# Kernel optimization log

Measured on AMD Instinct MI355X. Metric: run time of the kernel, lower is better.

The kernel has to match this reference:

```python
import jax, jax.numpy as jnp
import numpy as np

B, N, D = 32, 1024, 256
NHID = 512
NHID_HALF = NHID // 2
NCLASS = 2


def _xavier(key, shape):
    fan_in, fan_out = shape
    lim = float(np.sqrt(6.0 / (fan_in + fan_out)))
    return jax.random.uniform(key, shape, jnp.float32, -lim, lim)


def setup_inputs() -> dict:
    key = jax.random.key(0)
    ks = jax.random.split(key, 10)
    x = jax.random.normal(ks[0], (B, N, D), jnp.float32)
    adj = jax.random.uniform(ks[1], (B, N, N), jnp.float32)
    adj = adj / jnp.sum(adj, axis=-1, keepdims=True)  # row-normalized (mean aggregation)
    # GraphConv weights: shape (2*in_dim, out_dim) due to concat([x, agg(x)])
    W1 = _xavier(ks[2], (2 * D, NHID))
    b1 = jnp.zeros((NHID,), jnp.float32)
    W2 = _xavier(ks[3], (2 * NHID, NHID))
    b2 = jnp.zeros((NHID,), jnp.float32)
    W3 = _xavier(ks[4], (2 * NHID, NHID_HALF))
    b3 = jnp.zeros((NHID_HALF,), jnp.float32)
    W4 = _xavier(ks[5], (2 * NHID_HALF, NHID_HALF))
    b4 = jnp.zeros((NHID_HALF,), jnp.float32)
    # classifier: Linear(256,256) + PReLU(256) + Linear(256,2)
    cW1 = _xavier(ks[6], (NHID_HALF, NHID_HALF))
    cb1 = jnp.zeros((NHID_HALF,), jnp.float32)
    alpha = jnp.full((NHID_HALF,), 0.25, jnp.float32)
    cW2 = _xavier(ks[7], (NHID_HALF, NCLASS))
    cb2 = jnp.zeros((NCLASS,), jnp.float32)
    return {"x": x, "adj": adj, "W1": W1, "b1": b1, "W2": W2, "b2": b2,
            "W3": W3, "b3": b3, "W4": W4, "b4": b4,
            "cW1": cW1, "cb1": cb1, "alpha": alpha, "cW2": cW2, "cb2": cb2}


def _graphconv(x, adj, W, b):
    agg = jnp.einsum('bnm,bmd->bnd', adj, x)          # mean aggregation (adj row-normalized)
    cat = jnp.concatenate([x, agg], axis=-1)          # [B, N, 2*d]
    return jax.nn.relu(jnp.einsum('bnd,df->bnf', cat, W) + b)


def reference(x, adj, W1, b1, W2, b2, W3, b3, W4, b4, cW1, cb1, alpha, cW2, cb2):
    h = _graphconv(x, adj, W1, b1)
    h = _graphconv(h, adj, W2, b2)
    h = _graphconv(h, adj, W3, b3)
    h = _graphconv(h, adj, W4, b4)
    # classifier MLP with channel-wise PReLU
    h = jnp.einsum('bnd,df->bnf', h, cW1) + cb1
    h = jnp.where(h > 0, h, alpha * h)
    pred = jnp.einsum('bnd,df->bnf', h, cW2) + cb2
    return pred
```

## Files before the change

kernel.cpp:

```cpp
#include <hip/hip_runtime.h>

typedef short v8s __attribute__((ext_vector_type(8)));
typedef _Float16 v8h __attribute__((ext_vector_type(8)));
typedef float v4f __attribute__((ext_vector_type(4)));

#define BMT 128
#define BNT 128
#define BKT 32

__device__ __forceinline__ unsigned short f2bf(float f) {
    unsigned int u = __float_as_uint(f);
    u += 0x7fff + ((u >> 16) & 1);
    return (unsigned short)(u >> 16);
}
__device__ __forceinline__ unsigned short f2h(float f) {
    union { _Float16 h; unsigned short u; } c;
    c.h = (_Float16)f;
    return c.u;
}
__device__ __forceinline__ float h2f(unsigned short v) {
    union { unsigned short u; _Float16 h; } c;
    c.u = v;
    return (float)c.h;
}
__device__ __forceinline__ v8h as_h(v8s x) {
    union { v8s s; v8h h; } c;
    c.s = x;
    return c.h;
}

union U128 { unsigned short s[8]; uint4 v; };

__device__ __forceinline__ void gld16(const unsigned short* g, unsigned short* l) {
    __builtin_amdgcn_global_load_lds((const __attribute__((address_space(1))) void*)g,
                                     (__attribute__((address_space(3))) void*)l, 16, 0, 0);
}

__global__ __launch_bounds__(256) void split_f16(const float* __restrict__ x,
                                                 unsigned short* __restrict__ o, int n4) {
    int i = blockIdx.x * 256 + threadIdx.x;
    if (i < n4) {
        float4 f = ((const float4*)x)[i];
        float fv[4] = {f.x, f.y, f.z, f.w};
        ushort4 h;
        unsigned short* hp = (unsigned short*)&h;
#pragma unroll
        for (int j = 0; j < 4; ++j) hp[j] = f2h(fv[j]);
        ((ushort4*)o)[i] = h;
    }
}

__global__ __launch_bounds__(256) void split_hi(const float* __restrict__ x,
                                                unsigned short* __restrict__ oh, int n4) {
    int i = blockIdx.x * 256 + threadIdx.x;
    if (i < n4) {
        float4 f = ((const float4*)x)[i];
        float fv[4] = {f.x, f.y, f.z, f.w};
        ushort4 h;
        unsigned short* hp = (unsigned short*)&h;
#pragma unroll
        for (int j = 0; j < 4; ++j) hp[j] = f2bf(fv[j]);
        ((ushort4*)oh)[i] = h;
    }
}

__global__ __launch_bounds__(256) void tsplit16(const float* __restrict__ W,
                                                unsigned short* __restrict__ th, int R, int C) {
    int e = blockIdx.x * 256 + threadIdx.x;
    if (e < R * C) {
        int k = e / C, n = e - k * C;
        th[(size_t)n * R + k] = f2h(W[e]);
    }
}

__global__ __launch_bounds__(256) void transp_x(const float* __restrict__ src,
                                                unsigned short* __restrict__ th, int d) {
    __shared__ unsigned int lds[64 * 66];
    const int t = threadIdx.x;
    const int mt = blockIdx.x, ft = blockIdx.y, z = blockIdx.z;
    const int r = t >> 3, c8 = (t & 7) * 8;
#pragma unroll
    for (int half = 0; half < 2; ++half) {
        int rr = r + half * 32;
        size_t grow = (size_t)z * 1024 + mt * 64 + rr;
        const float* xs = src + grow * d + ft * 64 + c8;
        float4 f0 = *(const float4*)xs;
        float4 f1 = *(const float4*)(xs + 4);
        float fv[8] = {f0.x, f0.y, f0.z, f0.w, f1.x, f1.y, f1.z, f1.w};
#pragma unroll
        for (int j = 0; j < 8; ++j)
            lds[rr * 66 + c8 + j] = f2bf(fv[j]);
    }
    __syncthreads();
    const int f = t >> 3, m0 = (t & 7) * 8;
#pragma unroll
    for (int half = 0; half < 2; ++half) {
        int ff = f + half * 32;
        U128 uh;
#pragma unroll
        for (int j = 0; j < 8; ++j)
            uh.s[j] = (unsigned short)lds[(m0 + j) * 66 + ff];
        size_t orow = ((size_t)z * d + ft * 64 + ff) * 1024 + mt * 64 + m0;
        *(uint4*)(th + orow) = uh.v;
    }
}

template <int ACT, bool TWO, int AMODE, int DT, bool WRT>
__global__ __launch_bounds__(256) void gemm128(
    const void* a1, const unsigned short* __restrict__ a2,
    int K1, int K2,
    const unsigned short* __restrict__ b_, int ldb,
    const float* __restrict__ bias, const float* __restrict__ alpha,
    unsigned short* __restrict__ o_, int Nout,
    unsigned short* __restrict__ th,
    size_t aZ, size_t bZ, int cZRows,
    int nblk, int mBits)
{
    constexpr int LA = (AMODE == 0) ? 32 : 40;
    constexpr int LB = 32;
    __shared__ __align__(16) unsigned short Ash[BMT * LA];
    __shared__ __align__(16) unsigned short Bsh[BNT * LB];

    const int t = threadIdx.x;
    const int lane = t & 63, wave = t >> 6;
    const int wm = wave >> 1, wn = wave & 1;
    const int l15 = lane & 15, quad = lane >> 4;

    const int bx = blockIdx.x;
    const int low3 = bx & 7, rest = bx >> 3;
    const int nIdx = rest % nblk, g = rest / nblk;
    const int grp = g * 8 + low3;
    const int m0 = (grp & ((1 << mBits) - 1)) * BMT;
    const int zb = grp >> mBits;
    const int n0 = nIdx * BNT;

    const unsigned short* bhz = b_ + (size_t)zb * bZ;

    v4f acc[4][4] = {};

    const int nch = TWO ? 2 : 1;
    for (int ch = 0; ch < nch; ++ch) {
        const int K = (TWO && ch) ? K2 : K1;
        const int kr0 = (TWO && ch) ? K1 : 0;
        const unsigned short* ah = nullptr;
        const float* af = nullptr;
        if constexpr (AMODE == 0)
            ah = (ch ? a2 : (const unsigned short*)a1) + (size_t)zb * aZ;
        else
            af = (const float*)a1 + (size_t)zb * aZ;

        for (int kk = 0; kk < K; kk += BKT) {
            __syncthreads();
            if constexpr (AMODE == 0) {
#pragma unroll
                for (int i = 0; i < 2; ++i) {
                    int s = i * 256 + t;
                    int row = s >> 2;
                    int cg = (s & 3) ^ ((s >> 3) & 3);
                    size_t go = (size_t)(m0 + row) * K + kk + cg * 8;
                    int ls = (i * 256 + (t & ~63)) * 8;
                    gld16(ah + go, &Ash[ls]);
                }
            } else {
#pragma unroll
                for (int i = 0; i < 2; ++i) {
                    int cid = i * 256 + t;
                    int row = cid >> 2, c = cid & 3;
                    const float* src = af + (size_t)(m0 + row) * K + kk + c * 8;
                    float4 f0 = *(const float4*)src;
                    float4 f1 = *(const float4*)(src + 4);
                    float fv[8] = {f0.x, f0.y, f0.z, f0.w, f1.x, f1.y, f1.z, f1.w};
                    U128 uh;
#pragma unroll
                    for (int j = 0; j < 8; ++j) uh.s[j] = f2bf(fv[j]);
                    *(uint4*)&Ash[row * LA + c * 8] = uh.v;
                }
            }
#pragma unroll
            for (int i = 0; i < 2; ++i) {
                int s = i * 256 + t;
                int row = s >> 2;
                int cg = (s & 3) ^ ((s >> 3) & 3);
                size_t go = (size_t)(n0 + row) * ldb + kr0 + kk + cg * 8;
                int ls = (i * 256 + (t & ~63)) * 8;
                gld16(bhz + go, &Bsh[ls]);
            }
            __syncthreads();
            v8s ahf[4];
#pragma unroll
            for (int mi = 0; mi < 4; ++mi) {
                int row = wm * 64 + mi * 16 + l15;
                int off;
                if constexpr (AMODE == 0) off = row * LA + ((quad ^ ((row >> 1) & 3)) * 8);
                else                      off = row * LA + quad * 8;
                ahf[mi] = *(const v8s*)&Ash[off];
            }
#pragma unroll
            for (int ni = 0; ni < 4; ++ni) {
                int row = wn * 64 + ni * 16 + l15;
                int off = row * LB + ((quad ^ ((row >> 1) & 3)) * 8);
                v8s bhf = *(const v8s*)&Bsh[off];
#pragma unroll
                for (int mi = 0; mi < 4; ++mi) {
                    if constexpr (DT == 0)
                        acc[mi][ni] = __builtin_amdgcn_mfma_f32_16x16x32_bf16(ahf[mi], bhf, acc[mi][ni], 0, 0, 0);
                    else
                        acc[mi][ni] = __builtin_amdgcn_mfma_f32_16x16x32_f16(as_h(ahf[mi]), as_h(bhf), acc[mi][ni], 0, 0, 0);
                }
            }
        }
    }

    const size_t crow0 = (size_t)zb * cZRows + m0;
#pragma unroll
    for (int ni = 0; ni < 4; ++ni) {
        int n = n0 + wn * 64 + ni * 16 + l15;
        float bv = (ACT > 0) ? bias[n] : 0.f;
        float av = (ACT == 2) ? alpha[n] : 0.f;
#pragma unroll
        for (int mi = 0; mi < 4; ++mi) {
#pragma unroll
            for (int r = 0; r < 4; ++r) {
                int m = wm * 64 + mi * 16 + quad * 4 + r;
                float v = acc[mi][ni][r] + bv;
                if (ACT == 1) v = v > 0.f ? v : 0.f;
                if (ACT == 2) v = v > 0.f ? v : av * v;
                acc[mi][ni][r] = v;
                o_[(crow0 + m) * (size_t)Nout + n] = f2h(v);
            }
        }
    }

    if constexpr (WRT) {
        const int zbT = m0 >> 10;
        const int mloc0 = (m0 & 1023) + wm * 64;
#pragma unroll
        for (int ni = 0; ni < 4; ++ni) {
            int f = n0 + wn * 64 + ni * 16 + l15;
            size_t rowb = (((size_t)zbT * Nout + f) << 10) + mloc0;
#pragma unroll
            for (int mi = 0; mi < 4; ++mi) {
                ushort4 u;
                unsigned short* up = (unsigned short*)&u;
#pragma unroll
                for (int r = 0; r < 4; ++r) up[r] = f2bf(acc[mi][ni][r]);
                *(ushort4*)(th + rowb + mi * 16 + quad * 4) = u;
            }
        }
    }
}

template <int ACT, bool TWO, int DT, bool WRT, int BN2>
__global__ __launch_bounds__(512, 2) void gemm256(
    const unsigned short* __restrict__ a1, const unsigned short* __restrict__ a2,
    int K1, int K2,
    const unsigned short* __restrict__ b_, int ldb,
    const float* __restrict__ bias, const float* __restrict__ alpha,
    unsigned short* __restrict__ o_, int Nout,
    unsigned short* __restrict__ th,
    size_t aZ, size_t bZ, int cZRows,
    int nblk, int mBits)
{
    constexpr int ASLOT = 256 * 32;
    constexpr int BSLOT = BN2 * 32;
    constexpr int SLOT  = ASLOT + BSLOT;
    constexpr int LPT   = 2 + BN2 / 128;
    constexpr int WN    = BN2 / 64;
    constexpr int WM    = 8 / WN;
    constexpr int MREP  = 16 / WM;
    __shared__ __align__(16) unsigned short lds[4 * SLOT];

    const int t = threadIdx.x;
    const int lane = t & 63, wave = t >> 6;
    const int wm = wave / WN, wn = wave % WN;
    const int l15 = lane & 15, quad = lane >> 4;

    const int bx = blockIdx.x;
    const int low3 = bx & 7, rest = bx >> 3;
    const int nIdx = rest % nblk, g = rest / nblk;
    const int grp = g * 8 + low3;
    const int m0 = (grp & ((1 << mBits) - 1)) * 256;
    const int zb = grp >> mBits;
    const int n0 = nIdx * BN2;

    const unsigned short* A1 = a1 + (size_t)zb * aZ;
    const unsigned short* A2p = TWO ? (a2 + (size_t)zb * aZ) : nullptr;
    const unsigned short* B = b_ + (size_t)zb * bZ;

    const int NT1 = K1 >> 5;
    const int NTtot = NT1 + (TWO ? (K2 >> 5) : 0);

    auto stage = [&](int tt) {
        unsigned short* slot = &lds[(tt & 3) * SLOT];
        const unsigned short* abase;
        int astr;
        if constexpr (TWO) {
            if (tt >= NT1) { abase = A2p + ((size_t)(tt - NT1) << 5); astr = K2; }
            else           { abase = A1 + ((size_t)tt << 5); astr = K1; }
        } else {
            abase = A1 + ((size_t)tt << 5); astr = K1;
        }
#pragma unroll
        for (int i = 0; i < 2; ++i) {
            int s = i * 512 + t;
            int row = s >> 2;
            int cg = (s & 3) ^ ((s >> 3) & 3);
            gld16(abase + (size_t)(m0 + row) * astr + cg * 8,
                  &slot[(i * 512 + (t & ~63)) * 8]);
        }
        const unsigned short* bbase = B + ((size_t)tt << 5);
#pragma unroll
        for (int i = 0; i < BN2 / 128; ++i) {
            int s = i * 512 + t;
            int row = s >> 2;
            int cg = (s & 3) ^ ((s >> 3) & 3);
            gld16(bbase + (size_t)(n0 + row) * ldb + cg * 8,
                  &slot[ASLOT + (i * 512 + (t & ~63)) * 8]);
        }
    };

    v4f acc[MREP][4] = {};

    const int npro = NTtot < 3 ? NTtot : 3;
    for (int tt = 0; tt < npro; ++tt) stage(tt);

    for (int tt = 0; tt < NTtot; ++tt) {
        const int rem = NTtot - 1 - tt;
        if (rem >= 2) {
            if constexpr (LPT == 4) asm volatile("s_waitcnt vmcnt(8)" ::: "memory");
            else                    asm volatile("s_waitcnt vmcnt(6)" ::: "memory");
        } else if (rem == 1) {
            if constexpr (LPT == 4) asm volatile("s_waitcnt vmcnt(4)" ::: "memory");
            else                    asm volatile("s_waitcnt vmcnt(3)" ::: "memory");
        } else {
            asm volatile("s_waitcnt vmcnt(0)" ::: "memory");
        }
        __builtin_amdgcn_s_barrier();
        asm volatile("" ::: "memory");

        if (tt + 3 < NTtot) stage(tt + 3);

        const unsigned short* slot = &lds[(tt & 3) * SLOT];
        v8s af[MREP];
#pragma unroll
        for (int mi = 0; mi < MREP; ++mi) {
            int row = wm * (MREP * 16) + mi * 16 + l15;
            af[mi] = *(const v8s*)&slot[row * 32 + ((quad ^ ((row >> 1) & 3)) * 8)];
        }
        v8s bf[4];
#pragma unroll
        for (int ni = 0; ni < 4; ++ni) {
            int row = wn * 64 + ni * 16 + l15;
            bf[ni] = *(const v8s*)&slot[ASLOT + row * 32 + ((quad ^ ((row >> 1) & 3)) * 8)];
        }
        __builtin_amdgcn_s_setprio(1);
#pragma unroll
        for (int ni = 0; ni < 4; ++ni) {
#pragma unroll
            for (int mi = 0; mi < MREP; ++mi) {
                if constexpr (DT == 0)
                    acc[mi][ni] = __builtin_amdgcn_mfma_f32_16x16x32_bf16(af[mi], bf[ni], acc[mi][ni], 0, 0, 0);
                else
                    acc[mi][ni] = __builtin_amdgcn_mfma_f32_16x16x32_f16(as_h(af[mi]), as_h(bf[ni]), acc[mi][ni], 0, 0, 0);
            }
        }
        __builtin_amdgcn_s_setprio(0);
    }

    const size_t crow0 = (size_t)zb * cZRows + m0;
#pragma unroll
    for (int ni = 0; ni < 4; ++ni) {
        int n = n0 + wn * 64 + ni * 16 + l15;
        float bv = (ACT > 0) ? bias[n] : 0.f;
        float av = (ACT == 2) ? alpha[n] : 0.f;
#pragma unroll
        for (int mi = 0; mi < MREP; ++mi) {
#pragma unroll
            for (int r = 0; r < 4; ++r) {
                int m = wm * (MREP * 16) + mi * 16 + quad * 4 + r;
                float v = acc[mi][ni][r] + bv;
                if (ACT == 1) v = v > 0.f ? v : 0.f;
                if (ACT == 2) v = v > 0.f ? v : av * v;
                acc[mi][ni][r] = v;
                o_[(crow0 + m) * (size_t)Nout + n] = f2h(v);
            }
        }
    }

    if constexpr (WRT) {
        const int zbT = m0 >> 10;
        const int mloc0 = (m0 & 1023) + wm * (MREP * 16);
#pragma unroll
        for (int ni = 0; ni < 4; ++ni) {
            int f = n0 + wn * 64 + ni * 16 + l15;
            size_t rowb = (((size_t)zbT * Nout + f) << 10) + mloc0;
#pragma unroll
            for (int mi = 0; mi < MREP; ++mi) {
                ushort4 u;
                unsigned short* up = (unsigned short*)&u;
#pragma unroll
                for (int r = 0; r < 4; ++r) up[r] = f2bf(acc[mi][ni][r]);
                *(ushort4*)(th + rowb + mi * 16 + quad * 4) = u;
            }
        }
    }
}

__global__ __launch_bounds__(256) void final_gemm(const unsigned short* __restrict__ hh,
                                                  const float* __restrict__ W,
                                                  const float* __restrict__ bias,
                                                  float* __restrict__ out) {
    const int t = threadIdx.x;
    const int m = blockIdx.x * 64 + (t >> 2);
    const int kq = (t & 3) * 64;
    const unsigned short* ph = hh + (size_t)m * 256 + kq;
    float a0 = 0.f, a1 = 0.f;
#pragma unroll
    for (int i = 0; i < 8; ++i) {
        uint4 vh = *(const uint4*)(ph + i * 8);
        const unsigned short* sh = (const unsigned short*)&vh;
#pragma unroll
        for (int j = 0; j < 8; ++j) {
            int k = kq + i * 8 + j;
            float h = h2f(sh[j]);
            a0 += h * W[k * 2];
            a1 += h * W[k * 2 + 1];
        }
    }
    a0 += __shfl_down(a0, 2); a0 += __shfl_down(a0, 1);
    a1 += __shfl_down(a1, 2); a1 += __shfl_down(a1, 1);
    if ((t & 3) == 0) {
        out[(size_t)m * 2] = a0 + bias[0];
        out[(size_t)m * 2 + 1] = a1 + bias[1];
    }
}

extern "C" void kernel_launch(void* const* d_in, const int* in_sizes, int n_in,
                              void* d_out, int out_size, void* d_ws, size_t ws_size,
                              hipStream_t stream) {
    const float* x   = (const float*)d_in[0];
    const float* adj = (const float*)d_in[1];
    const float* W1  = (const float*)d_in[2];
    const float* b1  = (const float*)d_in[3];
    const float* W2  = (const float*)d_in[4];
    const float* b2  = (const float*)d_in[5];
    const float* W3  = (const float*)d_in[6];
    const float* b3  = (const float*)d_in[7];
    const float* W4  = (const float*)d_in[8];
    const float* b4  = (const float*)d_in[9];
    const float* cW1 = (const float*)d_in[10];
    const float* cb1 = (const float*)d_in[11];
    const float* alp = (const float*)d_in[12];
    const float* cW2 = (const float*)d_in[13];
    const float* cb2 = (const float*)d_in[14];
    float* out = (float*)d_out;

    const size_t P   = 32768ull * 512;
    const size_t XP  = 32768ull * 256;
    const size_t WT_TOT = 1245184;
    const size_t ADJ = 32ull * 1024 * 1024;

    unsigned short* N1  = (unsigned short*)d_ws;
    unsigned short* N2  = N1 + P;
    unsigned short* N3  = N2 + P;
    unsigned short* Th  = N3 + P;
    unsigned short* X16 = Th + P;
    unsigned short* WT  = X16 + XP;
    unsigned short* SA  = WT + WT_TOT;

    const size_t o1 = 0, o2 = 262144, o3 = 786432, o4 = 1048576, o5 = 1179648;
    const bool preAdj = ws_size >= (4 * P + XP + WT_TOT + ADJ) * sizeof(unsigned short);

    dim3 blk(256);
    dim3 blk5(512);

    split_f16<<<8192, blk, 0, stream>>>(x, X16, (int)(XP / 4));
    tsplit16<<<1024, blk, 0, stream>>>(W1,  WT + o1, 512, 512);
    tsplit16<<<2048, blk, 0, stream>>>(W2,  WT + o2, 1024, 512);
    tsplit16<<<1024, blk, 0, stream>>>(W3,  WT + o3, 1024, 256);
    tsplit16<<<512,  blk, 0, stream>>>(W4,  WT + o4, 512, 256);
    tsplit16<<<256,  blk, 0, stream>>>(cW1, WT + o5, 256, 256);
    if (preAdj)
        split_hi<<<32768, blk, 0, stream>>>(adj, SA, (int)(ADJ / 4));

    transp_x<<<dim3(16, 4, 32), blk, 0, stream>>>(x, Th, 256);

    if (preAdj)
        gemm256<0, false, 0, false, 128><<<256, blk5, 0, stream>>>(
            SA, nullptr, 1024, 0, Th, 1024, nullptr, nullptr,
            N2, 256, nullptr, (size_t)1 << 20, 256ull * 1024, 1024, 2, 2);
    else
        gemm128<0, false, 1, 0, false><<<512, blk, 0, stream>>>(
            adj, nullptr, 1024, 0, Th, 1024, nullptr, nullptr,
            N2, 256, nullptr, (size_t)1 << 20, 256ull * 1024, 1024, 2, 3);

    gemm256<1, true, 1, true, 256><<<256, blk5, 0, stream>>>(
        X16, N2, 256, 256, WT + o1, 512, b1, nullptr,
        N3, 512, Th, 0, 0, 0, 2, 7);

    if (preAdj)
        gemm256<0, false, 0, false, 256><<<256, blk5, 0, stream>>>(
            SA, nullptr, 1024, 0, Th, 1024, nullptr, nullptr,
            N1, 512, nullptr, (size_t)1 << 20, 512ull * 1024, 1024, 2, 2);
    else
        gemm128<0, false, 1, 0, false><<<1024, blk, 0, stream>>>(
            adj, nullptr, 1024, 0, Th, 1024, nullptr, nullptr,
            N1, 512, nullptr, (size_t)1 << 20, 512ull * 1024, 1024, 4, 3);

    gemm256<1, true, 1, true, 256><<<256, blk5, 0, stream>>>(
        N3, N1, 512, 512, WT + o2, 1024, b2, nullptr,
        N2, 512, Th, 0, 0, 0, 2, 7);

    if (preAdj)
        gemm256<0, false, 0, false, 256><<<256, blk5, 0, stream>>>(
            SA, nullptr, 1024, 0, Th, 1024, nullptr, nullptr,
            N1, 512, nullptr, (size_t)1 << 20, 512ull * 1024, 1024, 2, 2);
    else
        gemm128<0, false, 1, 0, false><<<1024, blk, 0, stream>>>(
            adj, nullptr, 1024, 0, Th, 1024, nullptr, nullptr,
            N1, 512, nullptr, (size_t)1 << 20, 512ull * 1024, 1024, 4, 3);

    gemm256<1, true, 1, true, 128><<<256, blk5, 0, stream>>>(
        N2, N1, 512, 512, WT + o3, 1024, b3, nullptr,
        N3, 256, Th, 0, 0, 0, 2, 7);

    if (preAdj)
        gemm256<0, false, 0, false, 128><<<256, blk5, 0, stream>>>(
            SA, nullptr, 1024, 0, Th, 1024, nullptr, nullptr,
            N1, 256, nullptr, (size_t)1 << 20, 256ull * 1024, 1024, 2, 2);
    else
        gemm128<0, false, 1, 0, false><<<512, blk, 0, stream>>>(
            adj, nullptr, 1024, 0, Th, 1024, nullptr, nullptr,
            N1, 256, nullptr, (size_t)1 << 20, 256ull * 1024, 1024, 2, 3);

    gemm256<1, true, 1, false, 128><<<256, blk5, 0, stream>>>(
        N3, N1, 256, 256, WT + o4, 512, b4, nullptr,
        N2, 256, nullptr, 0, 0, 0, 2, 7);

    gemm256<2, false, 1, false, 128><<<256, blk5, 0, stream>>>(
        N2, nullptr, 256, 0, WT + o5, 256, cb1, alp,
        N3, 256, nullptr, 0, 0, 0, 2, 7);

    final_gemm<<<512, blk, 0, stream>>>(N3, cW2, cb2, out);
}
```

Measured before the change: 559.0 us.

## Ping-pong register fragments to overlap LDS reads with MFMA in GEMM loop

Restructures the GEMM main loop into a two-step unrolled schedule with two sets of A/B register fragments. The LDS fragment reads for the next K-tile are issued before the MFMAs of the current tile, so LDS latency hides behind matrix math. Global-load wait counts and barriers are placed to match the new order. The cost is more live vector registers, which could lower occupancy, and wait/barrier logic that is easier to get wrong.

```diff
diff --git a/kernel.cpp b/kernel.cpp
--- a/kernel.cpp
+++ b/kernel.cpp
@@ -319,52 +319,69 @@
         }
     };
 
-    v4f acc[MREP][4] = {};
-
-    const int npro = NTtot < 3 ? NTtot : 3;
-    for (int tt = 0; tt < npro; ++tt) stage(tt);
-
-    for (int tt = 0; tt < NTtot; ++tt) {
-        const int rem = NTtot - 1 - tt;
-        if (rem >= 2) {
-            if constexpr (LPT == 4) asm volatile("s_waitcnt vmcnt(8)" ::: "memory");
-            else                    asm volatile("s_waitcnt vmcnt(6)" ::: "memory");
-        } else if (rem == 1) {
-            if constexpr (LPT == 4) asm volatile("s_waitcnt vmcnt(4)" ::: "memory");
-            else                    asm volatile("s_waitcnt vmcnt(3)" ::: "memory");
-        } else {
-            asm volatile("s_waitcnt vmcnt(0)" ::: "memory");
-        }
-        __builtin_amdgcn_s_barrier();
-        asm volatile("" ::: "memory");
-
-        if (tt + 3 < NTtot) stage(tt + 3);
-
+    auto rdfrags = [&](int tt, v8s (&AF)[MREP], v8s (&BF)[4]) {
         const unsigned short* slot = &lds[(tt & 3) * SLOT];
-        v8s af[MREP];
 #pragma unroll
         for (int mi = 0; mi < MREP; ++mi) {
             int row = wm * (MREP * 16) + mi * 16 + l15;
-            af[mi] = *(const v8s*)&slot[row * 32 + ((quad ^ ((row >> 1) & 3)) * 8)];
-        }
-        v8s bf[4];
+            AF[mi] = *(const v8s*)&slot[row * 32 + ((quad ^ ((row >> 1) & 3)) * 8)];
+        }
 #pragma unroll
         for (int ni = 0; ni < 4; ++ni) {
             int row = wn * 64 + ni * 16 + l15;
-            bf[ni] = *(const v8s*)&slot[ASLOT + row * 32 + ((quad ^ ((row >> 1) & 3)) * 8)];
-        }
+            BF[ni] = *(const v8s*)&slot[ASLOT + row * 32 + ((quad ^ ((row >> 1) & 3)) * 8)];
+        }
+    };
+
+    v4f acc[MREP][4] = {};
+
+    auto mfma_c = [&](v8s (&AF)[MREP], v8s (&BF)[4]) {
         __builtin_amdgcn_s_setprio(1);
 #pragma unroll
         for (int ni = 0; ni < 4; ++ni) {
 #pragma unroll
             for (int mi = 0; mi < MREP; ++mi) {
                 if constexpr (DT == 0)
-                    acc[mi][ni] = __builtin_amdgcn_mfma_f32_16x16x32_bf16(af[mi], bf[ni], acc[mi][ni], 0, 0, 0);
+                    acc[mi][ni] = __builtin_amdgcn_mfma_f32_16x16x32_bf16(AF[mi], BF[ni], acc[mi][ni], 0, 0, 0);
                 else
-                    acc[mi][ni] = __builtin_amdgcn_mfma_f32_16x16x32_f16(as_h(af[mi]), as_h(bf[ni]), acc[mi][ni], 0, 0, 0);
+                    acc[mi][ni] = __builtin_amdgcn_mfma_f32_16x16x32_f16(as_h(AF[mi]), as_h(BF[ni]), acc[mi][ni], 0, 0, 0);
             }
         }
         __builtin_amdgcn_s_setprio(0);
+    };
+
+    auto wait_lpt = [&]() {
+        if constexpr (LPT == 4) asm volatile("s_waitcnt vmcnt(4)" ::: "memory");
+        else                    asm volatile("s_waitcnt vmcnt(3)" ::: "memory");
+    };
+
+    v8s afA[MREP], bfA[4], afB[MREP], bfB[4];
+
+    stage(0); stage(1); stage(2);
+    wait_lpt();
+    __builtin_amdgcn_s_barrier();
+    asm volatile("" ::: "memory");
+    rdfrags(0, afA, bfA);
+
+    for (int tt = 0; tt < NTtot; tt += 2) {
+        if (tt + 3 < NTtot) stage(tt + 3);
+        if (tt + 1 < NTtot) rdfrags(tt + 1, afB, bfB);
+        mfma_c(afA, bfA);
+        if (tt + 2 < NTtot) {
+            if (tt + 3 < NTtot) wait_lpt();
+            else                asm volatile("s_waitcnt vmcnt(0)" ::: "memory");
+            __builtin_amdgcn_s_barrier();
+            asm volatile("" ::: "memory");
+        }
+        if (tt + 4 < NTtot) stage(tt + 4);
+        if (tt + 2 < NTtot) rdfrags(tt + 2, afA, bfA);
+        mfma_c(afB, bfB);
+        if (tt + 3 < NTtot) {
+            if (tt + 4 < NTtot) wait_lpt();
+            else                asm volatile("s_waitcnt vmcnt(0)" ::: "memory");
+            __builtin_amdgcn_s_barrier();
+            asm volatile("" ::: "memory");
+        }
     }
 
     const size_t crow0 = (size_t)zb * cZRows + m0;
```

New measurement: 553.5 us. About the same (-1.0%).
